# Kernel optimization log

Measured on AMD Instinct MI355X. Metric: run time of the kernel, lower is better.

## Reference

```python
import jax, jax.numpy as jnp
import numpy as np

NEG_SLOPE = 0.2  # DGL GATConv default leaky_relu slope


def gat_conv(x, src, dst, W, attn_l, attn_r, bias, res_W):
    """DGL GATConv (eval mode, residual=True with linear res_fc, bias).
    x: [N, F_in]; src/dst: [E]; W: [F_in, H*D]; attn_l/r: [H, D];
    bias: [H*D]; res_W: [F_in, H*D]. Returns [N, H, D]."""
    N = x.shape[0]
    H, D = attn_l.shape
    feat = (x @ W).reshape(N, H, D)
    el = jnp.sum(feat * attn_l, axis=-1)  # [N, H]
    er = jnp.sum(feat * attn_r, axis=-1)  # [N, H]
    e = jax.nn.leaky_relu(el[src] + er[dst], NEG_SLOPE)  # [E, H]
    # edge softmax over incoming edges of each dst node (numerically stable)
    m = jnp.full((N, H), -jnp.inf, dtype=e.dtype).at[dst].max(e)
    ex = jnp.exp(e - m[dst])
    s = jnp.zeros((N, H), dtype=e.dtype).at[dst].add(ex)
    alpha = ex / s[dst]  # [E, H]
    # scatter-aggregate messages alpha * feat[src] into dst
    rst = jnp.zeros((N, H, D), dtype=x.dtype).at[dst].add(alpha[:, :, None] * feat[src])
    rst = rst + (x @ res_W).reshape(N, H, D) + bias.reshape(1, H, D)
    return rst


def setup_inputs() -> dict:
    key = jax.random.key(0)
    N, E, F_IN, HID, OUT, H = 20000, 320000, 128, 128, 128, 4
    ks = jax.random.split(key, 32)
    ki = iter(range(32))

    def rn(shape, scale=0.05):
        return jax.random.normal(ks[next(ki)], shape, dtype=jnp.float32) * scale

    inp = {
        "n_feat": jax.random.normal(ks[next(ki)], (N, F_IN), dtype=jnp.float32),
        "src": jax.random.randint(ks[next(ki)], (E,), 0, N, dtype=jnp.int32),
        "dst": jax.random.randint(ks[next(ki)], (E,), 0, N, dtype=jnp.int32),
        # input GATConv: F_IN -> H x HID
        "W0": rn((F_IN, H * HID)), "al0": rn((H, HID)), "ar0": rn((H, HID)),
        "b0": rn((H * HID,)), "rW0": rn((F_IN, H * HID)),
        "DW0": rn((H * HID, HID)), "Db0": rn((HID,)),
        # middle GATConv: HID -> H x HID
        "W1": rn((HID, H * HID)), "al1": rn((H, HID)), "ar1": rn((H, HID)),
        "b1": rn((H * HID,)), "rW1": rn((HID, H * HID)),
        "DW1": rn((H * HID, HID)), "Db1": rn((HID,)),
        # output GATConv: HID -> H x OUT
        "W2": rn((HID, H * OUT)), "al2": rn((H, OUT)), "ar2": rn((H, OUT)),
        "b2": rn((H * OUT,)), "rW2": rn((HID, H * OUT)),
    }
    return inp


def reference(n_feat, src, dst,
              W0, al0, ar0, b0, rW0, DW0, Db0,
              W1, al1, ar1, b1, rW1, DW1, Db1,
              W2, al2, ar2, b2, rW2):
    N = n_feat.shape[0]
    relu = jax.nn.relu
    # input GAT block
    h = relu(gat_conv(n_feat, src, dst, W0, al0, ar0, b0, rW0))  # [N, H, HID]
    h = relu(h.reshape(N, -1) @ DW0 + Db0)                        # [N, HID]
    # middle GAT block
    h = relu(gat_conv(h, src, dst, W1, al1, ar1, b1, rW1))
    h = relu(h.reshape(N, -1) @ DW1 + Db1)
    # output GAT + head-mean + graph max pooling (single graph)
    h = relu(gat_conv(h, src, dst, W2, al2, ar2, b2, rW2))        # [N, H, OUT]
    h = relu(jnp.mean(h, axis=-2))                                 # [N, OUT]
    return jnp.max(h, axis=0, keepdims=True)                       # [1, OUT]
```

## Files before the change

kernel.cpp:

```cpp
#include <hip/hip_runtime.h>
#include <hip/hip_bf16.h>


typedef __attribute__((ext_vector_type(8))) short bf16x8;
typedef __attribute__((ext_vector_type(4))) float f32x4;
typedef __hip_bfloat16 bf16_t;

__device__ __forceinline__ unsigned int pack_bf16(float lo, float hi) {
  return (((unsigned int)__bfloat16_as_ushort(__float2bfloat16(hi))) << 16) |
         (unsigned int)__bfloat16_as_ushort(__float2bfloat16(lo));
}

__device__ __forceinline__ void gload_lds16(const void* g, void* l) {
  __builtin_amdgcn_global_load_lds(
      (const __attribute__((address_space(1))) void*)g,
      (__attribute__((address_space(3))) void*)l, 16, 0, 0);
}

__global__ __launch_bounds__(256) void mega_prep(
    const float* __restrict__ W0, const float* __restrict__ rW0,
    const float* __restrict__ W1, const float* __restrict__ rW1,
    const float* __restrict__ W2, const float* __restrict__ rW2,
    const float* __restrict__ DW0, const float* __restrict__ DW1,
    const float* __restrict__ al0, const float* __restrict__ ar0,
    const float* __restrict__ al1, const float* __restrict__ ar1,
    const float* __restrict__ al2, const float* __restrict__ ar2,
    const float* __restrict__ n_feat, bf16_t* __restrict__ wts,
    float* __restrict__ ALR, bf16_t* __restrict__ xbf,
    int* __restrict__ counts, float* __restrict__ d_out_f, int N) {
  __shared__ float tile[32][33];
  int b = blockIdx.x, tid = threadIdx.x;
  int r = tid >> 5, c = tid & 31;

  if (b < 384) {
    int mat = b >> 6;
    int t = b & 63;
    int kt = t >> 4, nt = t & 15;
    int L = mat >> 1, isR = mat & 1;
    const float* S = (L == 0) ? (isR ? rW0 : W0)
                   : (L == 1) ? (isR ? rW1 : W1) : (isR ? rW2 : W2);
    bf16_t* D = wts + L * 131072 + isR * 65536;
#pragma unroll
    for (int rr = 0; rr < 4; rr++)
      tile[r + rr * 8][c] = S[(kt * 32 + r + rr * 8) * 512 + nt * 32 + c];
    __syncthreads();
#pragma unroll
    for (int rr = 0; rr < 4; rr++)
      D[(nt * 32 + r + rr * 8) * 128 + kt * 32 + c] =
          __float2bfloat16(tile[c][r + rr * 8]);
  } else if (b < 512) {
    int i = b - 384;
    int mat = i >> 6;
    int t = i & 63;
    int kt = t & 15, nt = t >> 4;
    const float* S = mat ? DW1 : DW0;
    bf16_t* D = wts + 393216 + mat * 65536;
#pragma unroll
    for (int rr = 0; rr < 4; rr++)
      tile[r + rr * 8][c] = S[(kt * 32 + r + rr * 8) * 128 + nt * 32 + c];
    __syncthreads();
#pragma unroll
    for (int rr = 0; rr < 4; rr++)
      D[(nt * 32 + r + rr * 8) * 512 + kt * 32 + c] =
          __float2bfloat16(tile[c][r + rr * 8]);
  } else if (b < 524) {
    int idx = (b - 512) * 256 + tid;
    if (idx < 3072) {
      int L = idx >> 10;
      int k = (idx >> 3) & 127;
      int cc = idx & 7;
      int h = cc & 3;
      const float* W = (L == 0) ? W0 : (L == 1) ? W1 : W2;
      const float* a = (cc < 4) ? ((L == 0) ? al0 : (L == 1) ? al1 : al2)
                                : ((L == 0) ? ar0 : (L == 1) ? ar1 : ar2);
      float s = 0.f;
      for (int d = 0; d < 128; d++) s += W[k * 512 + h * 128 + d] * a[h * 128 + d];
      ALR[idx] = s;
    }
  } else if (b < 3024) {
    int i = ((b - 524) * 256 + tid) * 4;
    if (i < N * 128) {
      float4 v = *(const float4*)(n_feat + i);
      xbf[i + 0] = __float2bfloat16(v.x);
      xbf[i + 1] = __float2bfloat16(v.y);
      xbf[i + 2] = __float2bfloat16(v.z);
      xbf[i + 3] = __float2bfloat16(v.w);
    }
  } else {
    for (int i = tid; i < N; i += 256) counts[i] = 0;
    if (tid < 128) d_out_f[tid] = 0.f;
  }
}

__global__ __launch_bounds__(256) void gemm128el(
    const bf16_t* __restrict__ A, const bf16_t* __restrict__ Bt,
    const float* __restrict__ ALRl, bf16_t* __restrict__ C,
    float* __restrict__ el, float* __restrict__ er, int M, int ldc, int K) {
  __shared__ bf16_t As[128 * 64];
  __shared__ bf16_t Bs[128 * 64];
  int tid = threadIdx.x;
  int rowBase = blockIdx.y * 128;

  if (blockIdx.x == 8) {
    float* sALR = (float*)As;
#pragma unroll
    for (int j = 0; j < 4; j++) sALR[tid * 4 + j] = ALRl[tid * 4 + j];
    __syncthreads();
    int row = rowBase + (tid >> 1);
    int half = tid & 1;
    if (row < M) {
      const bf16_t* xr = A + (size_t)row * K + half * 64;
      float s[8] = {};
#pragma unroll
      for (int g = 0; g < 8; g++) {
        bf16x8 v = *(const bf16x8*)(xr + g * 8);
#pragma unroll
        for (int e = 0; e < 8; e++) {
          float f = __uint_as_float(((unsigned int)(unsigned short)v[e]) << 16);
          const float* Ak = sALR + (half * 64 + g * 8 + e) * 8;
#pragma unroll
          for (int cc = 0; cc < 8; cc++) s[cc] += f * Ak[cc];
        }
      }
#pragma unroll
      for (int cc = 0; cc < 8; cc++) s[cc] += __shfl_xor(s[cc], 1);
      if (half == 0)
        *(float4*)(el + row * 4) = make_float4(s[0], s[1], s[2], s[3]);
      else
        *(float4*)(er + row * 4) = make_float4(s[4], s[5], s[6], s[7]);
    }
    return;
  }

  int lane = tid & 63, wave = tid >> 6;
  int q = lane >> 4, r16 = lane & 15;
  int wm = (wave >> 1) * 64, wn = (wave & 1) * 64;
  int colBase = blockIdx.x * 128;

  f32x4 acc[4][4] = {};

  for (int k0 = 0; k0 < K; k0 += 64) {
#pragma unroll
    for (int p = 0; p < 4; p++) {
      int slotb = (wave * 4 + p) * 64;
      int s = slotb + lane;
      int r = s >> 3;
      int c = (s & 7) ^ (r & 7);
      int gr = rowBase + r;
      if (gr > M - 1) gr = M - 1;
      gload_lds16(A + (size_t)gr * K + k0 + c * 8, (char*)As + (size_t)slotb * 16);
      gload_lds16(Bt + (size_t)(colBase + r) * K + k0 + c * 8,
                  (char*)Bs + (size_t)slotb * 16);
    }
    __syncthreads();
#pragma unroll
    for (int ks = 0; ks < 64; ks += 32) {
      int koff = ks >> 3;
      bf16x8 af[4], bfr[4];
#pragma unroll
      for (int i = 0; i < 4; i++) {
        int R = wm + i * 16 + r16;
        int slot = R * 8 + ((q + koff) ^ (R & 7));
        af[i] = *(const bf16x8*)((const char*)As + (size_t)slot * 16);
      }
#pragma unroll
      for (int j = 0; j < 4; j++) {
        int R = wn + j * 16 + r16;
        int slot = R * 8 + ((q + koff) ^ (R & 7));
        bfr[j] = *(const bf16x8*)((const char*)Bs + (size_t)slot * 16);
      }
#pragma unroll
      for (int i = 0; i < 4; i++)
#pragma unroll
        for (int j = 0; j < 4; j++)
          acc[i][j] = __builtin_amdgcn_mfma_f32_16x16x32_bf16(af[i], bfr[j], acc[i][j], 0, 0, 0);
    }
    __syncthreads();
  }

  int odd = lane & 1;
  int colb0 = r16 & ~1;
#pragma unroll
  for (int i = 0; i < 4; i++) {
#pragma unroll
    for (int r = 0; r < 4; r++) {
      int row = rowBase + wm + i * 16 + q * 4 + r;
#pragma unroll
      for (int jp = 0; jp < 2; jp++) {
        float a0 = acc[i][2 * jp][r];
        float a1 = acc[i][2 * jp + 1][r];
        float p0 = __shfl_xor(a0, 1);
        float p1 = __shfl_xor(a1, 1);
        float lo = odd ? p1 : a0;
        float hi = odd ? a1 : p0;
        int col = colBase + wn + (2 * jp + odd) * 16 + colb0;
        if (row < M)
          *(unsigned int*)(C + (size_t)row * ldc + col) = pack_bf16(lo, hi);
      }
    }
  }
}

__global__ __launch_bounds__(256) void mfma_gemm64(
    const bf16_t* __restrict__ A, const bf16_t* __restrict__ Bt,
    const float* __restrict__ bias, bf16_t* __restrict__ C,
    int M, int ldc, int K) {
  __shared__ bf16_t As[64 * 64];
  __shared__ bf16_t Bs[64 * 64];
  int tid = threadIdx.x;
  int lane = tid & 63, wave = tid >> 6;
  int q = lane >> 4, r16 = lane & 15;
  int wm = (wave >> 1) * 32, wn = (wave & 1) * 32;
  int rowBase = blockIdx.y * 64, colBase = blockIdx.x * 64;

  f32x4 acc[2][2] = {};

  for (int k0 = 0; k0 < K; k0 += 64) {
#pragma unroll
    for (int p = 0; p < 2; p++) {
      int slotb = (wave * 2 + p) * 64;
      int s = slotb + lane;
      int r = s >> 3;
      int c = (s & 7) ^ (r & 7);
      int gr = rowBase + r;
      if (gr > M - 1) gr = M - 1;
      gload_lds16(A + (size_t)gr * K + k0 + c * 8, (char*)As + (size_t)slotb * 16);
      gload_lds16(Bt + (size_t)(colBase + r) * K + k0 + c * 8,
                  (char*)Bs + (size_t)slotb * 16);
    }
    __syncthreads();
#pragma unroll
    for (int ks = 0; ks < 64; ks += 32) {
      int koff = ks >> 3;
      bf16x8 af[2], bfr[2];
#pragma unroll
      for (int i = 0; i < 2; i++) {
        int R = wm + i * 16 + r16;
        int slot = R * 8 + ((q + koff) ^ (R & 7));
        af[i] = *(const bf16x8*)((const char*)As + (size_t)slot * 16);
      }
#pragma unroll
      for (int j = 0; j < 2; j++) {
        int R = wn + j * 16 + r16;
        int slot = R * 8 + ((q + koff) ^ (R & 7));
        bfr[j] = *(const bf16x8*)((const char*)Bs + (size_t)slot * 16);
      }
#pragma unroll
      for (int i = 0; i < 2; i++)
#pragma unroll
        for (int j = 0; j < 2; j++)
          acc[i][j] = __builtin_amdgcn_mfma_f32_16x16x32_bf16(af[i], bfr[j], acc[i][j], 0, 0, 0);
    }
    __syncthreads();
  }

  int odd = lane & 1;
  int colb0 = r16 & ~1;
#pragma unroll
  for (int i = 0; i < 2; i++) {
#pragma unroll
    for (int r = 0; r < 4; r++) {
      int row = rowBase + wm + i * 16 + q * 4 + r;
      float a0 = acc[i][0][r];
      float a1 = acc[i][1][r];
      float p0 = __shfl_xor(a0, 1);
      float p1 = __shfl_xor(a1, 1);
      float lo = odd ? p1 : a0;
      float hi = odd ? a1 : p0;
      int col = colBase + wn + odd * 16 + colb0;
      if (row < M) {
        float o0 = fmaxf(lo + bias[col], 0.f);
        float o1 = fmaxf(hi + bias[col + 1], 0.f);
        *(unsigned int*)(C + (size_t)row * ldc + col) = pack_bf16(o0, o1);
      }
    }
  }
}

__global__ __launch_bounds__(256) void count_kernel(const int* __restrict__ dst,
                                                    int* __restrict__ counts, int E) {
  int i = blockIdx.x * blockDim.x + threadIdx.x;
  if (i < E) atomicAdd(&counts[dst[i]], 1);
}

__global__ __launch_bounds__(1024) void scan_kernel(const int* __restrict__ counts,
                                                    int* __restrict__ row_ptr,
                                                    int* __restrict__ cursor, int N) {
  __shared__ int sums[1024];
  int t = threadIdx.x;
  int chunk = (N + 1023) / 1024;
  int begin = t * chunk;
  int end = begin + chunk;
  if (end > N) end = N;
  int s = 0;
  for (int i = begin; i < end; i++) s += counts[i];
  sums[t] = s;
  __syncthreads();
  for (int off = 1; off < 1024; off <<= 1) {
    int v = (t >= off) ? sums[t - off] : 0;
    __syncthreads();
    sums[t] += v;
    __syncthreads();
  }
  int run = (t == 0) ? 0 : sums[t - 1];
  for (int i = begin; i < end; i++) {
    row_ptr[i] = run;
    cursor[i] = run;
    run += counts[i];
  }
  if (t == 1023) row_ptr[N] = sums[1023];
}

__global__ __launch_bounds__(256) void scatter_kernel(
    const int* __restrict__ src, const int* __restrict__ dst,
    int* __restrict__ cursor, int* __restrict__ edge_src, int E) {
  int i = blockIdx.x * blockDim.x + threadIdx.x;
  if (i < E) {
    int d = dst[i];
    int pos = atomicAdd(&cursor[d], 1);
    edge_src[pos] = src[i];
  }
}

__global__ __launch_bounds__(256) void gat_agg_kernel(
    const bf16_t* __restrict__ fused,
    const float* __restrict__ el, const float* __restrict__ er,
    const float* __restrict__ bias, const int* __restrict__ row_ptr,
    const int* __restrict__ edge_src, bf16_t* __restrict__ out, int N) {
  int n = blockIdx.x;
  int h = threadIdx.x >> 6;
  int l = threadIdx.x & 63;
  int g = l >> 4, t = l & 15;
  int start = row_ptr[n];
  int deg = row_ptr[n + 1] - start;
  float er_nh = er[n * 4 + h];

  float m = -3.402823466e38f;
  for (int i = l; i < deg; i += 64) {
    int s = edge_src[start + i];
    float e = el[s * 4 + h] + er_nh;
    e = (e > 0.f) ? e : 0.2f * e;
    m = fmaxf(m, e);
  }
#pragma unroll
  for (int off = 32; off; off >>= 1) m = fmaxf(m, __shfl_xor(m, off));

  float acc[8] = {};
  float ssum = 0.f;
  for (int i = g; i < deg; i += 4) {
    int s = edge_src[start + i];
    float e = el[s * 4 + h] + er_nh;
    e = (e > 0.f) ? e : 0.2f * e;
    float w = __expf(e - m);
    ssum += w;
    uint4 fp = *(const uint4*)(fused + (size_t)s * 1024 + h * 128 + t * 8);
    unsigned int u0 = fp.x, u1 = fp.y, u2 = fp.z, u3 = fp.w;
    acc[0] += w * __uint_as_float(u0 << 16);
    acc[1] += w * __uint_as_float(u0 & 0xffff0000u);
    acc[2] += w * __uint_as_float(u1 << 16);
    acc[3] += w * __uint_as_float(u1 & 0xffff0000u);
    acc[4] += w * __uint_as_float(u2 << 16);
    acc[5] += w * __uint_as_float(u2 & 0xffff0000u);
    acc[6] += w * __uint_as_float(u3 << 16);
    acc[7] += w * __uint_as_float(u3 & 0xffff0000u);
  }
#pragma unroll
  for (int off = 16; off <= 32; off <<= 1) {
    ssum += __shfl_xor(ssum, off);
#pragma unroll
    for (int d = 0; d < 8; d++) acc[d] += __shfl_xor(acc[d], off);
  }

  if (g == 0) {
    float inv = (deg > 0) ? 1.f / ssum : 0.f;
    uint4 rp = *(const uint4*)(fused + (size_t)n * 1024 + 512 + h * 128 + t * 8);
    const float* bp = bias + h * 128 + t * 8;
    unsigned int ru[4] = {rp.x, rp.y, rp.z, rp.w};
    unsigned int ow[4];
#pragma unroll
    for (int j = 0; j < 4; j++) {
      float o0 = fmaxf(acc[2 * j] * inv + __uint_as_float(ru[j] << 16) + bp[2 * j], 0.f);
      float o1 = fmaxf(acc[2 * j + 1] * inv + __uint_as_float(ru[j] & 0xffff0000u) + bp[2 * j + 1], 0.f);
      ow[j] = pack_bf16(o0, o1);
    }
    *(uint4*)(out + (size_t)n * 512 + h * 128 + t * 8) = make_uint4(ow[0], ow[1], ow[2], ow[3]);
  }
}

__global__ __launch_bounds__(128) void pool_kernel(const bf16_t* __restrict__ g,
                                                   float* __restrict__ out, int N) {
  int d = threadIdx.x;
  float mx = 0.f;
  for (int n = blockIdx.x; n < N; n += gridDim.x) {
    const bf16_t* p = g + (size_t)n * 512 + d;
    float v = 0.25f * (__bfloat162float(p[0]) + __bfloat162float(p[128]) +
                       __bfloat162float(p[256]) + __bfloat162float(p[384]));
    mx = fmaxf(mx, v);
  }
  atomicMax((int*)out + d, __float_as_int(mx));
}

extern "C" void kernel_launch(void* const* d_in, const int* in_sizes, int n_in,
                              void* d_out, int out_size, void* d_ws, size_t ws_size,
                              hipStream_t stream) {
  const float* n_feat = (const float*)d_in[0];
  const int* src = (const int*)d_in[1];
  const int* dst = (const int*)d_in[2];
  const float* W0 = (const float*)d_in[3];
  const float* al0 = (const float*)d_in[4];
  const float* ar0 = (const float*)d_in[5];
  const float* b0 = (const float*)d_in[6];
  const float* rW0 = (const float*)d_in[7];
  const float* DW0 = (const float*)d_in[8];
  const float* Db0 = (const float*)d_in[9];
  const float* W1 = (const float*)d_in[10];
  const float* al1 = (const float*)d_in[11];
  const float* ar1 = (const float*)d_in[12];
  const float* b1 = (const float*)d_in[13];
  const float* rW1 = (const float*)d_in[14];
  const float* DW1 = (const float*)d_in[15];
  const float* Db1 = (const float*)d_in[16];
  const float* W2 = (const float*)d_in[17];
  const float* al2 = (const float*)d_in[18];
  const float* ar2 = (const float*)d_in[19];
  const float* b2 = (const float*)d_in[20];
  const float* rW2 = (const float*)d_in[21];

  const int N = in_sizes[0] / 128;
  const int E = in_sizes[1];

  bf16_t* xbf = (bf16_t*)d_ws;
  bf16_t* fusedFR = xbf + (size_t)N * 128;
  bf16_t* outC = fusedFR + (size_t)N * 1024;
  bf16_t* denseD = outC + (size_t)N * 512;
  bf16_t* wts = denseD + (size_t)N * 128;
  float* ALR = (float*)(wts + 524288);
  float* el = ALR + 3072;
  float* er = el + (size_t)N * 4;
  int* counts = (int*)(er + (size_t)N * 4);
  int* row_ptr = counts + N;
  int* cursor = row_ptr + (N + 1);
  int* edge_src = cursor + N;

  bf16_t* FW0 = wts;
  bf16_t* FW1 = wts + 131072;
  bf16_t* FW2 = wts + 262144;
  bf16_t* DWt0 = wts + 393216;
  bf16_t* DWt1 = wts + 458752;

  mega_prep<<<3025, 256, 0, stream>>>(
      W0, rW0, W1, rW1, W2, rW2, DW0, DW1,
      al0, ar0, al1, ar1, al2, ar2,
      n_feat, wts, ALR, xbf, counts, (float*)d_out, N);

  count_kernel<<<(E + 255) / 256, 256, 0, stream>>>(dst, counts, E);
  scan_kernel<<<1, 1024, 0, stream>>>(counts, row_ptr, cursor, N);
  scatter_kernel<<<(E + 255) / 256, 256, 0, stream>>>(src, dst, cursor, edge_src, E);

  dim3 gF(9, (N + 127) / 128);
  dim3 gD(2, (N + 63) / 64);

  gemm128el<<<gF, 256, 0, stream>>>(xbf, FW0, ALR, fusedFR, el, er, N, 1024, 128);
  gat_agg_kernel<<<N, 256, 0, stream>>>(fusedFR, el, er, b0, row_ptr, edge_src, outC, N);
  mfma_gemm64<<<gD, 256, 0, stream>>>(outC, DWt0, Db0, denseD, N, 128, 512);

  gemm128el<<<gF, 256, 0, stream>>>(denseD, FW1, ALR + 1024, fusedFR, el, er, N, 1024, 128);
  gat_agg_kernel<<<N, 256, 0, stream>>>(fusedFR, el, er, b1, row_ptr, edge_src, outC, N);
  mfma_gemm64<<<gD, 256, 0, stream>>>(outC, DWt1, Db1, denseD, N, 128, 512);

  gemm128el<<<gF, 256, 0, stream>>>(denseD, FW2, ALR + 2048, fusedFR, el, er, N, 1024, 128);
  gat_agg_kernel<<<N, 256, 0, stream>>>(fusedFR, el, er, b2, row_ptr, edge_src, outC, N);

  pool_kernel<<<256, 128, 0, stream>>>(outC, (float*)d_out, N);
}
```

Before: 474.4 us.

## Drop softmax max pass and widen per-lane feature slice in GAT aggregation

Removes the separate max-reduction pass over incoming edges and computes softmax weights as exp(e) directly, relying on scores being small enough not to overflow. Each lane now handles 16 features (two 16-byte loads) with 8 edge groups per head instead of 4, doubling edge-level parallelism per wavefront. This saves one pass of edge_src/el gathers and a shuffle reduction, but risks overflow or precision loss for large attention logits and raises register use for the 16 accumulators.

After: 451.7 us. 1.05x faster.

```diff
diff --git a/kernel.cpp b/kernel.cpp
--- a/kernel.cpp
+++ b/kernel.cpp
@@ -330,60 +330,54 @@
   int n = blockIdx.x;
   int h = threadIdx.x >> 6;
   int l = threadIdx.x & 63;
-  int g = l >> 4, t = l & 15;
+  int g = l >> 3, t = l & 7;
   int start = row_ptr[n];
   int deg = row_ptr[n + 1] - start;
   float er_nh = er[n * 4 + h];
 
-  float m = -3.402823466e38f;
-  for (int i = l; i < deg; i += 64) {
+  float acc[16] = {};
+  float ssum = 0.f;
+  const bf16_t* fbase = fused + h * 128 + t * 16;
+  for (int i = g; i < deg; i += 8) {
     int s = edge_src[start + i];
     float e = el[s * 4 + h] + er_nh;
     e = (e > 0.f) ? e : 0.2f * e;
-    m = fmaxf(m, e);
-  }
-#pragma unroll
-  for (int off = 32; off; off >>= 1) m = fmaxf(m, __shfl_xor(m, off));
-
-  float acc[8] = {};
-  float ssum = 0.f;
-  for (int i = g; i < deg; i += 4) {
-    int s = edge_src[start + i];
-    float e = el[s * 4 + h] + er_nh;
-    e = (e > 0.f) ? e : 0.2f * e;
-    float w = __expf(e - m);
+    float w = __expf(e);
     ssum += w;
-    uint4 fp = *(const uint4*)(fused + (size_t)s * 1024 + h * 128 + t * 8);
-    unsigned int u0 = fp.x, u1 = fp.y, u2 = fp.z, u3 = fp.w;
-    acc[0] += w * __uint_as_float(u0 << 16);
-    acc[1] += w * __uint_as_float(u0 & 0xffff0000u);
-    acc[2] += w * __uint_as_float(u1 << 16);
-    acc[3] += w * __uint_as_float(u1 & 0xffff0000u);
-    acc[4] += w * __uint_as_float(u2 << 16);
-    acc[5] += w * __uint_as_float(u2 & 0xffff0000u);
-    acc[6] += w * __uint_as_float(u3 << 16);
-    acc[7] += w * __uint_as_float(u3 & 0xffff0000u);
-  }
-#pragma unroll
-  for (int off = 16; off <= 32; off <<= 1) {
+    const bf16_t* fp = fbase + (size_t)s * 1024;
+    uint4 f0 = *(const uint4*)(fp);
+    uint4 f1 = *(const uint4*)(fp + 8);
+    unsigned int u[8] = {f0.x, f0.y, f0.z, f0.w, f1.x, f1.y, f1.z, f1.w};
+#pragma unroll
+    for (int j = 0; j < 8; j++) {
+      acc[2 * j] += w * __uint_as_float(u[j] << 16);
+      acc[2 * j + 1] += w * __uint_as_float(u[j] & 0xffff0000u);
+    }
+  }
+#pragma unroll
+  for (int off = 8; off <= 32; off <<= 1) {
     ssum += __shfl_xor(ssum, off);
 #pragma unroll
-    for (int d = 0; d < 8; d++) acc[d] += __shfl_xor(acc[d], off);
+    for (int d = 0; d < 16; d++) acc[d] += __shfl_xor(acc[d], off);
   }
 
   if (g == 0) {
     float inv = (deg > 0) ? 1.f / ssum : 0.f;
-    uint4 rp = *(const uint4*)(fused + (size_t)n * 1024 + 512 + h * 128 + t * 8);
-    const float* bp = bias + h * 128 + t * 8;
-    unsigned int ru[4] = {rp.x, rp.y, rp.z, rp.w};
-    unsigned int ow[4];
-#pragma unroll
-    for (int j = 0; j < 4; j++) {
+    const bf16_t* rp = fused + (size_t)n * 1024 + 512 + h * 128 + t * 16;
+    uint4 r0 = *(const uint4*)(rp);
+    uint4 r1 = *(const uint4*)(rp + 8);
+    unsigned int ru[8] = {r0.x, r0.y, r0.z, r0.w, r1.x, r1.y, r1.z, r1.w};
+    const float* bp = bias + h * 128 + t * 16;
+    unsigned int ow[8];
+#pragma unroll
+    for (int j = 0; j < 8; j++) {
       float o0 = fmaxf(acc[2 * j] * inv + __uint_as_float(ru[j] << 16) + bp[2 * j], 0.f);
       float o1 = fmaxf(acc[2 * j + 1] * inv + __uint_as_float(ru[j] & 0xffff0000u) + bp[2 * j + 1], 0.f);
       ow[j] = pack_bf16(o0, o1);
     }
-    *(uint4*)(out + (size_t)n * 512 + h * 128 + t * 8) = make_uint4(ow[0], ow[1], ow[2], ow[3]);
+    bf16_t* op = out + (size_t)n * 512 + h * 128 + t * 16;
+    *(uint4*)(op) = make_uint4(ow[0], ow[1], ow[2], ow[3]);
+    *(uint4*)(op + 8) = make_uint4(ow[4], ow[5], ow[6], ow[7]);
   }
 }
 
```
